# Kernel optimization log

Hardware: AMD Instinct MI355X
Metric: run time of the kernel (lower is better)

## Reference

```python
import jax, jax.numpy as jnp
import numpy as np

# Dimensions
O, D, F_LSOA = 128, 128, 64      # origins, destinations, LSOA feature dim
T, FE, H = 128, 16, 64           # max seq len, edge_feature_dim, gru_hidden
NH, NO, PH = 128, 64, 128        # node_hidden, node_out, pair_hidden
P = O * D                        # number of O-D pairs


def _mlp3(x, W1, b1, W2, b2, W3, b3):
    # Linear->ReLU->Linear->ReLU->Linear (dropout is identity in eval mode)
    h = jax.nn.relu(x @ W1 + b1)
    h = jax.nn.relu(h @ W2 + b2)
    return h @ W3 + b3


def setup_inputs() -> dict:
    key = jax.random.key(0)
    ks = jax.random.split(key, 32)

    def rn(k, shape, s):
        return jax.random.normal(k, shape, dtype=jnp.float32) * s

    inp = {
        "O_feats": rn(ks[0], (O, F_LSOA), 1.0),
        "D_feats": rn(ks[1], (D, F_LSOA), 1.0),
        "seqs": rn(ks[2], (P, T, FE), 1.0),
        "lengths": jax.random.randint(ks[3], (P,), 1, T + 1, dtype=jnp.int32),
        # enc_O
        "WO1": rn(ks[4], (F_LSOA, NH), 0.05), "bO1": jnp.zeros((NH,), jnp.float32),
        "WO2": rn(ks[5], (NH, NH), 0.05),     "bO2": jnp.zeros((NH,), jnp.float32),
        "WO3": rn(ks[6], (NH, NO), 0.05),     "bO3": jnp.zeros((NO,), jnp.float32),
        # enc_D
        "WD1": rn(ks[7], (F_LSOA, NH), 0.05), "bD1": jnp.zeros((NH,), jnp.float32),
        "WD2": rn(ks[8], (NH, NH), 0.05),     "bD2": jnp.zeros((NH,), jnp.float32),
        "WD3": rn(ks[9], (NH, NO), 0.05),     "bD3": jnp.zeros((NO,), jnp.float32),
        # pair_head: 2*node_out -> pair_hidden -> 1
        "Wp1": rn(ks[10], (2 * NO, PH), 0.05), "bp1": jnp.zeros((PH,), jnp.float32),
        "Wp2": rn(ks[11], (PH, 1), 0.05),      "bp2": jnp.zeros((1,), jnp.float32),
        # GRU (gate order r, z, n as in PyTorch)
        "W_ih": rn(ks[12], (FE, 3 * H), 0.1),  "b_ih": jnp.zeros((3 * H,), jnp.float32),
        "W_hh": rn(ks[13], (H, 3 * H), 0.1),   "b_hh": jnp.zeros((3 * H,), jnp.float32),
        # seq_head
        "Ws": rn(ks[14], (H, 1), 0.1),         "bs": jnp.zeros((1,), jnp.float32),
    }
    return inp


def reference(O_feats, D_feats, seqs, lengths,
              WO1, bO1, WO2, bO2, WO3, bO3,
              WD1, bD1, WD2, bD2, WD3, bD3,
              Wp1, bp1, Wp2, bp2,
              W_ih, W_hh, b_ih, b_hh,
              Ws, bs):
    # Node encoders
    eo = _mlp3(O_feats, WO1, bO1, WO2, bO2, WO3, bO3)   # [O, NO]
    ed = _mlp3(D_feats, WD1, bD1, WD2, bD2, WD3, bD3)   # [D, NO]

    # Pairwise score: concat(eo, ed) -> MLP -> softplus
    pair_in = jnp.concatenate([
        jnp.broadcast_to(eo[:, None, :], (O, D, NO)),
        jnp.broadcast_to(ed[None, :, :], (O, D, NO)),
    ], axis=-1)                                          # [O, D, 2*NO]
    hp = jax.nn.relu(pair_in @ Wp1 + bp1)                # [O, D, PH]
    z_pair = (hp @ Wp2 + bp2)[..., 0]                    # [O, D]
    s_pair = jax.nn.softplus(z_pair)

    # Length-masked GRU over all O*D padded sequences (equiv. to pack_padded)
    xT = jnp.swapaxes(seqs, 0, 1)                        # [T, P, FE]
    h0 = jnp.zeros((P, H), jnp.float32)

    def step(h, inp):
        xt, t = inp
        gx = xt @ W_ih + b_ih                            # [P, 3H]
        gh = h @ W_hh + b_hh                             # [P, 3H]
        xr, xz, xn = jnp.split(gx, 3, axis=-1)
        hr, hz, hn = jnp.split(gh, 3, axis=-1)
        r = jax.nn.sigmoid(xr + hr)
        zg = jax.nn.sigmoid(xz + hz)
        n = jnp.tanh(xn + r * hn)
        h_new = (1.0 - zg) * n + zg * h
        h = jnp.where((t < lengths)[:, None], h_new, h)  # freeze past seq end
        return h, None

    h_last, _ = jax.lax.scan(step, h0, (xT, jnp.arange(T)))  # [P, H]

    p_seq = jax.nn.sigmoid(h_last @ Ws + bs)[:, 0].reshape(O, D)
    return jnp.sum(s_pair * p_seq)
```

## Files before the change

### kernel.cpp

```cpp
#include <hip/hip_runtime.h>
#include <hip/hip_bf16.h>

#define O_N 128
#define D_N 128
#define F_LS 64
#define T_MAX 128
#define FE_N 16
#define H_GRU 64
#define NH 128
#define NO 64
#define PH 128
#define NG 1024

typedef _Float16 f16;
typedef f16 f16x4 __attribute__((ext_vector_type(4)));
typedef f16 f16x8 __attribute__((ext_vector_type(8)));
typedef float f32x4 __attribute__((ext_vector_type(4)));

__device__ __forceinline__ float fast_sigmoid(float x) {
    return __builtin_amdgcn_rcpf(1.f + __expf(-x));
}

__global__ __launch_bounds__(128) void k_enc(
    const float* __restrict__ O_feats, const float* __restrict__ D_feats,
    const float* __restrict__ WO1, const float* __restrict__ bO1,
    const float* __restrict__ WO2, const float* __restrict__ bO2,
    const float* __restrict__ WO3, const float* __restrict__ bO3,
    const float* __restrict__ WD1, const float* __restrict__ bD1,
    const float* __restrict__ WD2, const float* __restrict__ bD2,
    const float* __restrict__ WD3, const float* __restrict__ bD3,
    const float* __restrict__ Wp1,
    float* __restrict__ PA, float* __restrict__ PB, float* __restrict__ d_out)
{
    __shared__ float h1[NH];
    __shared__ float h2[NH];
    __shared__ float ev[NO];
    const int b = blockIdx.x;
    const int enc = b >> 7;
    const int row = b & 127;
    const int t = threadIdx.x;
    if (b == 0 && t == 0) d_out[0] = 0.f;

    const float* x  = (enc ? D_feats : O_feats) + row * F_LS;
    const float* W1 = enc ? WD1 : WO1;  const float* b1 = enc ? bD1 : bO1;
    const float* W2 = enc ? WD2 : WO2;  const float* b2 = enc ? bD2 : bO2;
    const float* W3 = enc ? WD3 : WO3;  const float* b3 = enc ? bD3 : bO3;

    float a = b1[t];
    #pragma unroll 8
    for (int k = 0; k < F_LS; ++k) a += x[k] * W1[k * NH + t];
    h1[t] = fmaxf(a, 0.f);
    __syncthreads();

    a = b2[t];
    #pragma unroll 8
    for (int k = 0; k < NH; ++k) a += h1[k] * W2[k * NH + t];
    h2[t] = fmaxf(a, 0.f);
    __syncthreads();

    if (t < NO) {
        a = b3[t];
        #pragma unroll 8
        for (int k = 0; k < NH; ++k) a += h2[k] * W3[k * NO + t];
        ev[t] = a;
    }
    __syncthreads();

    const float* Wp = Wp1 + (enc ? NO * PH : 0);
    a = 0.f;
    #pragma unroll 8
    for (int k = 0; k < NO; ++k) a += ev[k] * Wp[k * PH + t];
    (enc ? PB : PA)[row * PH + t] = a;
}

__global__ __launch_bounds__(128) void k_pair(
    const float* __restrict__ PA, const float* __restrict__ PB,
    const float* __restrict__ bp1, const float* __restrict__ Wp2,
    const float* __restrict__ bp2, float* __restrict__ s_pair)
{
    const int i = blockIdx.x;
    const int j = threadIdx.x;
    __shared__ float pa[PH];
    __shared__ float b1s[PH];
    __shared__ float w2s[PH];
    pa[j]  = PA[i * PH + j];
    b1s[j] = bp1[j];
    w2s[j] = Wp2[j];
    __syncthreads();
    const float* pb = PB + j * PH;
    float acc = 0.f;
    #pragma unroll 8
    for (int c = 0; c < PH; ++c)
        acc += w2s[c] * fmaxf(pa[c] + pb[c] + b1s[c], 0.f);
    float z = acc + bp2[0];
    float sp = fmaxf(z, 0.f) + log1pf(__expf(-fabsf(z)));
    s_pair[i * 128 + j] = sp;
}

__global__ __launch_bounds__(1024) void k_sort(
    const int* __restrict__ lengths, int* __restrict__ perm)
{
    __shared__ int cnt[130];
    __shared__ int suf[130];
    const int t = threadIdx.x;
    if (t < 130) cnt[t] = 0;
    __syncthreads();
    for (int i = t; i < 16384; i += 1024) atomicAdd(&cnt[lengths[i]], 1);
    __syncthreads();
    if (t < 130) suf[t] = cnt[t];
    __syncthreads();
    for (int d = 1; d < 130; d <<= 1) {
        int v = 0;
        if (t < 130) { v = suf[t]; if (t + d < 130) v += suf[t + d]; }
        __syncthreads();
        if (t < 130) suf[t] = v;
        __syncthreads();
    }
    if (t < 129) cnt[t] = (t + 1 < 130) ? suf[t + 1] : 0;
    __syncthreads();
    for (int i = t; i < 16384; i += 1024) {
        int pos = atomicAdd(&cnt[lengths[i]], 1);
        perm[pos] = i;
    }
}

__global__ __launch_bounds__(256, 4) void k_gru(
    const float* __restrict__ seqs, const int* __restrict__ lengths,
    const int* __restrict__ perm,
    const float* __restrict__ W_ih, const float* __restrict__ b_ih,
    const float* __restrict__ W_hh, const float* __restrict__ b_hh,
    const float* __restrict__ Ws, const float* __restrict__ bs,
    const float* __restrict__ s_pair, float* __restrict__ d_out)
{
    __shared__ __align__(16) f16 hbuf[2][16 * 72];
    __shared__ float red[64];
    const int tid = threadIdx.x;
    const int w  = tid >> 6;
    const int l  = tid & 63;
    const int q  = l >> 4;
    const int n  = l & 15;
    const int c  = w * 16 + n;
    const int colbase = w * 16 + q * 4;
    const int pb = blockIdx.x * 16;
    const float S_RZ = -1.4426950408889634f;
    const float S_N  =  2.8853900817779268f;

    f16x8 wh[3][2], wi[3];
    #pragma unroll
    for (int g = 0; g < 3; ++g) {
        const int gb = g * 64;
        const float s = (g < 2) ? S_RZ : S_N;
        #pragma unroll
        for (int ks = 0; ks < 2; ++ks)
            #pragma unroll
            for (int j = 0; j < 8; ++j)
                wh[g][ks][j] = (f16)(W_hh[(ks * 32 + q * 8 + j) * 192 + gb + c] * s);
        #pragma unroll
        for (int j = 0; j < 8; ++j) {
            int k = q * 8 + j;
            wi[g][j] = (k < FE_N) ? (f16)(W_ih[k * 192 + gb + c] * s) : (f16)0.f;
        }
    }
    f32x4 c_r, c_z, c_hn, c_xn;
    float wsc[4];
    #pragma unroll
    for (int r = 0; r < 4; ++r) {
        int col = colbase + r;
        c_r[r]  = S_RZ * (b_ih[col] + b_hh[col]);
        c_z[r]  = S_RZ * (b_ih[64 + col] + b_hh[64 + col]);
        c_hn[r] = S_N * b_hh[128 + col];
        c_xn[r] = S_N * b_ih[128 + col];
        wsc[r]  = Ws[col];
    }
    const int myp   = perm[pb + n];
    const int mylen = lengths[myp];
    int ml = mylen;
    ml = max(ml, __shfl_xor(ml, 1));
    ml = max(ml, __shfl_xor(ml, 2));
    ml = max(ml, __shfl_xor(ml, 4));
    ml = max(ml, __shfl_xor(ml, 8));
    const int maxlen = __builtin_amdgcn_readfirstlane(ml);

    {
        f16x8 z8 = {(f16)0, (f16)0, (f16)0, (f16)0, (f16)0, (f16)0, (f16)0, (f16)0};
        if (tid < 144) *(f16x8*)&hbuf[0][tid * 8] = z8;
    }

    const float4* xp = (const float4*)(seqs + (size_t)myp * (T_MAX * FE_N)) + q * 2;
    float4 xa = {0.f, 0.f, 0.f, 0.f}, xb = xa;
    if (q < 2) { xa = xp[0]; xb = xp[1]; }

    float hold[4] = {0.f, 0.f, 0.f, 0.f};
    const f16x8 zero8 = {(f16)0, (f16)0, (f16)0, (f16)0, (f16)0, (f16)0, (f16)0, (f16)0};
    __syncthreads();

    #pragma unroll 1
    for (int t = 0; t < maxlen; t += 2) {
        #pragma unroll
        for (int sub = 0; sub < 2; ++sub) {
            const int tt = t + sub;
            if (sub == 1 && tt >= maxlen) break;
            const f16* hb  = hbuf[sub];
            f16*       hbw = hbuf[sub ^ 1];

            f16x8 ax = zero8;
            if (q < 2) {
                ax[0] = (f16)xa.x; ax[1] = (f16)xa.y; ax[2] = (f16)xa.z; ax[3] = (f16)xa.w;
                ax[4] = (f16)xb.x; ax[5] = (f16)xb.y; ax[6] = (f16)xb.z; ax[7] = (f16)xb.w;
                int tn = (tt + 1 < maxlen) ? (tt + 1) : tt;
                xa = xp[tn * 4];
                xb = xp[tn * 4 + 1];
            }
            f16x8 bh0 = *(const f16x8*)&hb[n * 72 + 8 * q];
            f16x8 bh1 = *(const f16x8*)&hb[n * 72 + 32 + 8 * q];

            f32x4 ar = __builtin_amdgcn_mfma_f32_16x16x32_f16(wh[0][0], bh0, c_r, 0, 0, 0);
            ar = __builtin_amdgcn_mfma_f32_16x16x32_f16(wh[0][1], bh1, ar, 0, 0, 0);
            ar = __builtin_amdgcn_mfma_f32_16x16x32_f16(wi[0],    ax,  ar, 0, 0, 0);
            f32x4 az = __builtin_amdgcn_mfma_f32_16x16x32_f16(wh[1][0], bh0, c_z, 0, 0, 0);
            az = __builtin_amdgcn_mfma_f32_16x16x32_f16(wh[1][1], bh1, az, 0, 0, 0);
            az = __builtin_amdgcn_mfma_f32_16x16x32_f16(wi[1],    ax,  az, 0, 0, 0);
            f32x4 hn = __builtin_amdgcn_mfma_f32_16x16x32_f16(wh[2][0], bh0, c_hn, 0, 0, 0);
            hn = __builtin_amdgcn_mfma_f32_16x16x32_f16(wh[2][1], bh1, hn, 0, 0, 0);
            f32x4 xn = __builtin_amdgcn_mfma_f32_16x16x32_f16(wi[2], ax, c_xn, 0, 0, 0);

            const bool live = (tt < mylen);
            #pragma unroll
            for (int r = 0; r < 4; ++r) {
                float rg    = __builtin_amdgcn_rcpf(1.f + __builtin_amdgcn_exp2f(ar[r]));
                float zg    = __builtin_amdgcn_rcpf(1.f + __builtin_amdgcn_exp2f(az[r]));
                float inner = fmaf(rg, hn[r], xn[r]);
                float nn    = fmaf(-2.f, __builtin_amdgcn_rcpf(1.f + __builtin_amdgcn_exp2f(inner)), 1.f);
                float hnew  = fmaf(zg, hold[r] - nn, nn);
                hold[r] = live ? hnew : hold[r];
            }
            f16x4 hv4;
            hv4[0] = (f16)hold[0];
            hv4[1] = (f16)hold[1];
            hv4[2] = (f16)hold[2];
            hv4[3] = (f16)hold[3];
            *(f16x4*)&hbw[n * 72 + colbase] = hv4;
            __syncthreads();
        }
    }

    float part = hold[0] * wsc[0] + hold[1] * wsc[1] +
                 hold[2] * wsc[2] + hold[3] * wsc[3];
    part += __shfl_xor(part, 16);
    part += __shfl_xor(part, 32);
    if (l < 16) red[w * 16 + n] = part;
    __syncthreads();
    if (tid < 16) {
        float s = red[tid] + red[16 + tid] + red[32 + tid] + red[48 + tid];
        float pv = fast_sigmoid(s + bs[0]);
        float contrib = s_pair[perm[pb + tid]] * pv;
        #pragma unroll
        for (int off = 1; off < 16; off <<= 1)
            contrib += __shfl_xor(contrib, off);
        if (tid == 0) atomicAdd(d_out, contrib);
    }
}

extern "C" void kernel_launch(void* const* d_in, const int* in_sizes, int n_in,
                              void* d_out, int out_size, void* d_ws, size_t ws_size,
                              hipStream_t stream)
{
    const float* O_feats = (const float*)d_in[0];
    const float* D_feats = (const float*)d_in[1];
    const float* seqs    = (const float*)d_in[2];
    const int*   lengths = (const int*)d_in[3];
    const float* WO1 = (const float*)d_in[4];  const float* bO1 = (const float*)d_in[5];
    const float* WO2 = (const float*)d_in[6];  const float* bO2 = (const float*)d_in[7];
    const float* WO3 = (const float*)d_in[8];  const float* bO3 = (const float*)d_in[9];
    const float* WD1 = (const float*)d_in[10]; const float* bD1 = (const float*)d_in[11];
    const float* WD2 = (const float*)d_in[12]; const float* bD2 = (const float*)d_in[13];
    const float* WD3 = (const float*)d_in[14]; const float* bD3 = (const float*)d_in[15];
    const float* Wp1 = (const float*)d_in[16]; const float* bp1 = (const float*)d_in[17];
    const float* Wp2 = (const float*)d_in[18]; const float* bp2 = (const float*)d_in[19];
    const float* W_ih = (const float*)d_in[20]; const float* b_ih = (const float*)d_in[21];
    const float* W_hh = (const float*)d_in[22]; const float* b_hh = (const float*)d_in[23];
    const float* Ws   = (const float*)d_in[24]; const float* bs   = (const float*)d_in[25];

    float* out    = (float*)d_out;
    float* PA     = (float*)d_ws;
    float* PB     = PA + 128 * 128;
    float* s_pair = PB + 128 * 128;
    int*   perm   = (int*)(s_pair + 16384);

    k_enc<<<256, 128, 0, stream>>>(O_feats, D_feats,
                                   WO1, bO1, WO2, bO2, WO3, bO3,
                                   WD1, bD1, WD2, bD2, WD3, bD3,
                                   Wp1, PA, PB, out);
    k_pair<<<128, 128, 0, stream>>>(PA, PB, bp1, Wp2, bp2, s_pair);
    k_sort<<<1, 1024, 0, stream>>>(lengths, perm);
    k_gru<<<1024, 256, 0, stream>>>(seqs, lengths, perm, W_ih, b_ih, W_hh, b_hh,
                                    Ws, bs, s_pair, out);
}
```

Baseline: 367.0 us.

## Run each GRU tile in a single wavefront to drop block barriers

Moves the whole 16-sequence GRU tile into one 64-thread wavefront. Each lane now holds the weights for all four 16-column output tiles, so the per-step __syncthreads and the double-buffered LDS hidden state go away. The r/z/xn biases are folded into the input MFMA through a constant-one input element. The cost is four times the serial MFMA and activation work per wave and fewer resident waves per CU to hide MFMA and transcendental latency.

```diff
diff --git a/kernel.cpp b/kernel.cpp
--- a/kernel.cpp
+++ b/kernel.cpp
@@ -10,7 +10,6 @@
 #define NH 128
 #define NO 64
 #define PH 128
-#define NG 1024
 
 typedef _Float16 f16;
 typedef f16 f16x4 __attribute__((ext_vector_type(4)));
@@ -124,7 +123,7 @@
     }
 }
 
-__global__ __launch_bounds__(256, 4) void k_gru(
+__global__ __launch_bounds__(64, 1) void k_gru(
     const float* __restrict__ seqs, const int* __restrict__ lengths,
     const int* __restrict__ perm,
     const float* __restrict__ W_ih, const float* __restrict__ b_ih,
@@ -132,46 +131,49 @@
     const float* __restrict__ Ws, const float* __restrict__ bs,
     const float* __restrict__ s_pair, float* __restrict__ d_out)
 {
-    __shared__ __align__(16) f16 hbuf[2][16 * 72];
-    __shared__ float red[64];
+    __shared__ __align__(16) f16 hbuf[16 * 72];
     const int tid = threadIdx.x;
-    const int w  = tid >> 6;
-    const int l  = tid & 63;
-    const int q  = l >> 4;
-    const int n  = l & 15;
-    const int c  = w * 16 + n;
-    const int colbase = w * 16 + q * 4;
+    const int q = tid >> 4;
+    const int n = tid & 15;
     const int pb = blockIdx.x * 16;
     const float S_RZ = -1.4426950408889634f;
     const float S_N  =  2.8853900817779268f;
 
-    f16x8 wh[3][2], wi[3];
+    f16x8 wh[3][4][2], wi[3][4];
+    f32x4 c_hn[4];
     #pragma unroll
     for (int g = 0; g < 3; ++g) {
-        const int gb = g * 64;
         const float s = (g < 2) ? S_RZ : S_N;
         #pragma unroll
-        for (int ks = 0; ks < 2; ++ks)
+        for (int mt = 0; mt < 4; ++mt) {
+            const int col = g * 64 + mt * 16 + n;
             #pragma unroll
-            for (int j = 0; j < 8; ++j)
-                wh[g][ks][j] = (f16)(W_hh[(ks * 32 + q * 8 + j) * 192 + gb + c] * s);
-        #pragma unroll
-        for (int j = 0; j < 8; ++j) {
-            int k = q * 8 + j;
-            wi[g][j] = (k < FE_N) ? (f16)(W_ih[k * 192 + gb + c] * s) : (f16)0.f;
+            for (int ks = 0; ks < 2; ++ks)
+                #pragma unroll
+                for (int j = 0; j < 8; ++j)
+                    wh[g][mt][ks][j] = (f16)(W_hh[(ks * 32 + q * 8 + j) * 192 + col] * s);
+            #pragma unroll
+            for (int j = 0; j < 8; ++j) {
+                const int k = q * 8 + j;
+                float v = 0.f;
+                if (k < FE_N) {
+                    v = W_ih[k * 192 + col] * s;
+                } else if (k == FE_N) {
+                    const int c0 = mt * 16 + n;
+                    v = (g == 0) ? S_RZ * (b_ih[c0] + b_hh[c0])
+                      : (g == 1) ? S_RZ * (b_ih[64 + c0] + b_hh[64 + c0])
+                                 : S_N * b_ih[128 + c0];
+                }
+                wi[g][mt][j] = (f16)v;
+            }
         }
     }
-    f32x4 c_r, c_z, c_hn, c_xn;
-    float wsc[4];
     #pragma unroll
-    for (int r = 0; r < 4; ++r) {
-        int col = colbase + r;
-        c_r[r]  = S_RZ * (b_ih[col] + b_hh[col]);
-        c_z[r]  = S_RZ * (b_ih[64 + col] + b_hh[64 + col]);
-        c_hn[r] = S_N * b_hh[128 + col];
-        c_xn[r] = S_N * b_ih[128 + col];
-        wsc[r]  = Ws[col];
-    }
+    for (int mt = 0; mt < 4; ++mt)
+        #pragma unroll
+        for (int r = 0; r < 4; ++r)
+            c_hn[mt][r] = S_N * b_hh[128 + mt * 16 + q * 4 + r];
+
     const int myp   = perm[pb + n];
     const int mylen = lengths[myp];
     int ml = mylen;
@@ -182,78 +184,80 @@
     const int maxlen = __builtin_amdgcn_readfirstlane(ml);
 
     {
-        f16x8 z8 = {(f16)0, (f16)0, (f16)0, (f16)0, (f16)0, (f16)0, (f16)0, (f16)0};
-        if (tid < 144) *(f16x8*)&hbuf[0][tid * 8] = z8;
+        f16x8 z8 = {};
+        #pragma unroll
+        for (int i = 0; i < 3; ++i) {
+            int idx = tid + i * 64;
+            if (idx < 144) *(f16x8*)&hbuf[idx * 8] = z8;
+        }
     }
 
     const float4* xp = (const float4*)(seqs + (size_t)myp * (T_MAX * FE_N)) + q * 2;
-    float4 xa = {0.f, 0.f, 0.f, 0.f}, xb = xa;
-    if (q < 2) { xa = xp[0]; xb = xp[1]; }
-
-    float hold[4] = {0.f, 0.f, 0.f, 0.f};
-    const f16x8 zero8 = {(f16)0, (f16)0, (f16)0, (f16)0, (f16)0, (f16)0, (f16)0, (f16)0};
-    __syncthreads();
-
-    #pragma unroll 1
-    for (int t = 0; t < maxlen; t += 2) {
-        #pragma unroll
-        for (int sub = 0; sub < 2; ++sub) {
-            const int tt = t + sub;
-            if (sub == 1 && tt >= maxlen) break;
-            const f16* hb  = hbuf[sub];
-            f16*       hbw = hbuf[sub ^ 1];
-
-            f16x8 ax = zero8;
-            if (q < 2) {
-                ax[0] = (f16)xa.x; ax[1] = (f16)xa.y; ax[2] = (f16)xa.z; ax[3] = (f16)xa.w;
-                ax[4] = (f16)xb.x; ax[5] = (f16)xb.y; ax[6] = (f16)xb.z; ax[7] = (f16)xb.w;
-                int tn = (tt + 1 < maxlen) ? (tt + 1) : tt;
-                xa = xp[tn * 4];
-                xb = xp[tn * 4 + 1];
-            }
-            f16x8 bh0 = *(const f16x8*)&hb[n * 72 + 8 * q];
-            f16x8 bh1 = *(const f16x8*)&hb[n * 72 + 32 + 8 * q];
-
-            f32x4 ar = __builtin_amdgcn_mfma_f32_16x16x32_f16(wh[0][0], bh0, c_r, 0, 0, 0);
-            ar = __builtin_amdgcn_mfma_f32_16x16x32_f16(wh[0][1], bh1, ar, 0, 0, 0);
-            ar = __builtin_amdgcn_mfma_f32_16x16x32_f16(wi[0],    ax,  ar, 0, 0, 0);
-            f32x4 az = __builtin_amdgcn_mfma_f32_16x16x32_f16(wh[1][0], bh0, c_z, 0, 0, 0);
-            az = __builtin_amdgcn_mfma_f32_16x16x32_f16(wh[1][1], bh1, az, 0, 0, 0);
-            az = __builtin_amdgcn_mfma_f32_16x16x32_f16(wi[1],    ax,  az, 0, 0, 0);
-            f32x4 hn = __builtin_amdgcn_mfma_f32_16x16x32_f16(wh[2][0], bh0, c_hn, 0, 0, 0);
-            hn = __builtin_amdgcn_mfma_f32_16x16x32_f16(wh[2][1], bh1, hn, 0, 0, 0);
-            f32x4 xn = __builtin_amdgcn_mfma_f32_16x16x32_f16(wi[2], ax, c_xn, 0, 0, 0);
-
-            const bool live = (tt < mylen);
+    float4 x0a = {0.f, 0.f, 0.f, 0.f}, x0b = x0a, x1a = x0a, x1b = x0a;
+    if (q < 2) {
+        x0a = xp[0]; x0b = xp[1];
+        x1a = xp[4]; x1b = xp[5];
+    }
+    f16x8 ax = {};
+    if (q == 2) ax[0] = (f16)1.f;
+    const f32x4 zc = {0.f, 0.f, 0.f, 0.f};
+    float hold[4][4] = {};
+
+    auto step = [&](int TT, float4& XA, float4& XB) {
+        f16x8 bh0 = *(const f16x8*)&hbuf[n * 72 + 8 * q];
+        f16x8 bh1 = *(const f16x8*)&hbuf[n * 72 + 32 + 8 * q];
+        if (q < 2) {
+            ax[0] = (f16)XA.x; ax[1] = (f16)XA.y;
+            ax[2] = (f16)XA.z; ax[3] = (f16)XA.w;
+            ax[4] = (f16)XB.x; ax[5] = (f16)XB.y;
+            ax[6] = (f16)XB.z; ax[7] = (f16)XB.w;
+            int tn = (TT + 2 < maxlen) ? (TT + 2) : (maxlen - 1);
+            XA = xp[tn * 4]; XB = xp[tn * 4 + 1];
+        }
+        const bool live = (TT < mylen);
+        #pragma unroll
+        for (int mt = 0; mt < 4; ++mt) {
+            f32x4 ar = __builtin_amdgcn_mfma_f32_16x16x32_f16(wh[0][mt][0], bh0, zc, 0, 0, 0);
+            ar = __builtin_amdgcn_mfma_f32_16x16x32_f16(wh[0][mt][1], bh1, ar, 0, 0, 0);
+            ar = __builtin_amdgcn_mfma_f32_16x16x32_f16(wi[0][mt],    ax,  ar, 0, 0, 0);
+            f32x4 az = __builtin_amdgcn_mfma_f32_16x16x32_f16(wh[1][mt][0], bh0, zc, 0, 0, 0);
+            az = __builtin_amdgcn_mfma_f32_16x16x32_f16(wh[1][mt][1], bh1, az, 0, 0, 0);
+            az = __builtin_amdgcn_mfma_f32_16x16x32_f16(wi[1][mt],    ax,  az, 0, 0, 0);
+            f32x4 hn = __builtin_amdgcn_mfma_f32_16x16x32_f16(wh[2][mt][0], bh0, c_hn[mt], 0, 0, 0);
+            hn = __builtin_amdgcn_mfma_f32_16x16x32_f16(wh[2][mt][1], bh1, hn, 0, 0, 0);
+            f32x4 xn = __builtin_amdgcn_mfma_f32_16x16x32_f16(wi[2][mt], ax, zc, 0, 0, 0);
+            f16x4 hv4;
             #pragma unroll
             for (int r = 0; r < 4; ++r) {
                 float rg    = __builtin_amdgcn_rcpf(1.f + __builtin_amdgcn_exp2f(ar[r]));
                 float zg    = __builtin_amdgcn_rcpf(1.f + __builtin_amdgcn_exp2f(az[r]));
                 float inner = fmaf(rg, hn[r], xn[r]);
                 float nn    = fmaf(-2.f, __builtin_amdgcn_rcpf(1.f + __builtin_amdgcn_exp2f(inner)), 1.f);
-                float hnew  = fmaf(zg, hold[r] - nn, nn);
-                hold[r] = live ? hnew : hold[r];
+                float hnew  = fmaf(zg, hold[mt][r] - nn, nn);
+                hold[mt][r] = live ? hnew : hold[mt][r];
+                hv4[r] = (f16)hold[mt][r];
             }
-            f16x4 hv4;
-            hv4[0] = (f16)hold[0];
-            hv4[1] = (f16)hold[1];
-            hv4[2] = (f16)hold[2];
-            hv4[3] = (f16)hold[3];
-            *(f16x4*)&hbw[n * 72 + colbase] = hv4;
-            __syncthreads();
+            *(f16x4*)&hbuf[n * 72 + mt * 16 + 4 * q] = hv4;
         }
-    }
-
-    float part = hold[0] * wsc[0] + hold[1] * wsc[1] +
-                 hold[2] * wsc[2] + hold[3] * wsc[3];
+    };
+
+    #pragma unroll 1
+    for (int t = 0; t < maxlen; t += 2) {
+        step(t, x0a, x0b);
+        if (t + 1 < maxlen) step(t + 1, x1a, x1b);
+    }
+
+    float part = 0.f;
+    #pragma unroll
+    for (int mt = 0; mt < 4; ++mt)
+        #pragma unroll
+        for (int r = 0; r < 4; ++r)
+            part += hold[mt][r] * Ws[mt * 16 + q * 4 + r];
     part += __shfl_xor(part, 16);
     part += __shfl_xor(part, 32);
-    if (l < 16) red[w * 16 + n] = part;
-    __syncthreads();
     if (tid < 16) {
-        float s = red[tid] + red[16 + tid] + red[32 + tid] + red[48 + tid];
-        float pv = fast_sigmoid(s + bs[0]);
-        float contrib = s_pair[perm[pb + tid]] * pv;
+        float pv = fast_sigmoid(part + bs[0]);
+        float contrib = s_pair[myp] * pv;
         #pragma unroll
         for (int off = 1; off < 16; off <<= 1)
             contrib += __shfl_xor(contrib, off);
@@ -293,6 +297,6 @@
                                    Wp1, PA, PB, out);
     k_pair<<<128, 128, 0, stream>>>(PA, PB, bp1, Wp2, bp2, s_pair);
     k_sort<<<1, 1024, 0, stream>>>(lengths, perm);
-    k_gru<<<1024, 256, 0, stream>>>(seqs, lengths, perm, W_ih, b_ih, W_hh, b_hh,
-                                    Ws, bs, s_pair, out);
-}
+    k_gru<<<1024, 64, 0, stream>>>(seqs, lengths, perm, W_ih, b_ih, W_hh, b_hh,
+                                   Ws, bs, s_pair, out);
+}
```

Measured after the change: 408.2 us. 1.11x slower.

## Pack four GRU sequence groups per 1024-thread block with deeper input prefetch

Applied to the files above, without the earlier changes.

Each GRU workgroup now holds four independent 16-sequence groups: 16 waves, 1024 threads, 256 blocks. The loop is bounded by the block's longest sequence, and each group skips steps past its own sorted max length. The seqs input is now prefetched two steps ahead into separate per-sub-step registers. The input-projection MFMAs are issued before the hidden-state ones, and f16 packing uses cvt_pkrtz. The risks are that barriers now span 16 waves, so groups with shorter sequences sit idle, and that launch_bounds(1024,4) may squeeze the VGPR budget and cause spills.

```diff
diff --git a/kernel.cpp b/kernel.cpp
--- a/kernel.cpp
+++ b/kernel.cpp
@@ -10,9 +10,10 @@
 #define NH 128
 #define NO 64
 #define PH 128
-#define NG 1024
+#define ENG 4
 
 typedef _Float16 f16;
+typedef __fp16 hf2 __attribute__((ext_vector_type(2)));
 typedef f16 f16x4 __attribute__((ext_vector_type(4)));
 typedef f16 f16x8 __attribute__((ext_vector_type(8)));
 typedef float f32x4 __attribute__((ext_vector_type(4)));
@@ -124,7 +125,7 @@
     }
 }
 
-__global__ __launch_bounds__(256, 4) void k_gru(
+__global__ __launch_bounds__(1024, 4) void k_gru(
     const float* __restrict__ seqs, const int* __restrict__ lengths,
     const int* __restrict__ perm,
     const float* __restrict__ W_ih, const float* __restrict__ b_ih,
@@ -132,16 +133,18 @@
     const float* __restrict__ Ws, const float* __restrict__ bs,
     const float* __restrict__ s_pair, float* __restrict__ d_out)
 {
-    __shared__ __align__(16) f16 hbuf[2][16 * 72];
-    __shared__ float red[64];
+    __shared__ __align__(16) f16 hbuf[ENG][2][16 * 72];
+    __shared__ float red[ENG][64];
     const int tid = threadIdx.x;
-    const int w  = tid >> 6;
+    const int wave = tid >> 6;
+    const int e = wave >> 2;
+    const int wi_ = wave & 3;
     const int l  = tid & 63;
     const int q  = l >> 4;
     const int n  = l & 15;
-    const int c  = w * 16 + n;
-    const int colbase = w * 16 + q * 4;
-    const int pb = blockIdx.x * 16;
+    const int c  = wi_ * 16 + n;
+    const int colbase = wi_ * 16 + q * 4;
+    const int pb = blockIdx.x * 64 + e * 16;
     const float S_RZ = -1.4426950408889634f;
     const float S_N  =  2.8853900817779268f;
 
@@ -174,90 +177,93 @@
     }
     const int myp   = perm[pb + n];
     const int mylen = lengths[myp];
-    int ml = mylen;
-    ml = max(ml, __shfl_xor(ml, 1));
-    ml = max(ml, __shfl_xor(ml, 2));
-    ml = max(ml, __shfl_xor(ml, 4));
-    ml = max(ml, __shfl_xor(ml, 8));
-    const int maxlen = __builtin_amdgcn_readfirstlane(ml);
+    const int elen  = lengths[perm[pb]];
+    const int blen  = lengths[perm[blockIdx.x * 64]];
 
     {
-        f16x8 z8 = {(f16)0, (f16)0, (f16)0, (f16)0, (f16)0, (f16)0, (f16)0, (f16)0};
-        if (tid < 144) *(f16x8*)&hbuf[0][tid * 8] = z8;
+        f16x8 z8 = {};
+        f16* hb = (f16*)hbuf;
+        #pragma unroll 2
+        for (int i = tid; i < 1152; i += 1024) *(f16x8*)&hb[i * 8] = z8;
     }
 
     const float4* xp = (const float4*)(seqs + (size_t)myp * (T_MAX * FE_N)) + q * 2;
-    float4 xa = {0.f, 0.f, 0.f, 0.f}, xb = xa;
-    if (q < 2) { xa = xp[0]; xb = xp[1]; }
-
+    float4 x0a = {0.f, 0.f, 0.f, 0.f}, x0b = x0a, x1a = x0a, x1b = x0a;
+    if (q < 2) {
+        x0a = xp[0]; x0b = xp[1];
+        x1a = xp[4]; x1b = xp[5];
+    }
+    f16x8 ax = {};
     float hold[4] = {0.f, 0.f, 0.f, 0.f};
-    const f16x8 zero8 = {(f16)0, (f16)0, (f16)0, (f16)0, (f16)0, (f16)0, (f16)0, (f16)0};
-    __syncthreads();
+    __syncthreads();
+
+    auto step = [&](int TT, int sub, float4& XA, float4& XB) {
+        const f16* hb  = hbuf[e][sub];
+        f16*       hbw = hbuf[e][sub ^ 1];
+        f16x8 bh0 = *(const f16x8*)&hb[n * 72 + 8 * q];
+        f16x8 bh1 = *(const f16x8*)&hb[n * 72 + 32 + 8 * q];
+        if (q < 2) {
+            union { f16x8 v8; hf2 v2[4]; } u;
+            u.v2[0] = __builtin_amdgcn_cvt_pkrtz(XA.x, XA.y);
+            u.v2[1] = __builtin_amdgcn_cvt_pkrtz(XA.z, XA.w);
+            u.v2[2] = __builtin_amdgcn_cvt_pkrtz(XB.x, XB.y);
+            u.v2[3] = __builtin_amdgcn_cvt_pkrtz(XB.z, XB.w);
+            ax = u.v8;
+            int tn = (TT + 2 < elen) ? (TT + 2) : (elen - 1);
+            XA = xp[tn * 4]; XB = xp[tn * 4 + 1];
+        }
+        f32x4 ar = __builtin_amdgcn_mfma_f32_16x16x32_f16(wi[0], ax, c_r, 0, 0, 0);
+        f32x4 az = __builtin_amdgcn_mfma_f32_16x16x32_f16(wi[1], ax, c_z, 0, 0, 0);
+        f32x4 xn = __builtin_amdgcn_mfma_f32_16x16x32_f16(wi[2], ax, c_xn, 0, 0, 0);
+        ar = __builtin_amdgcn_mfma_f32_16x16x32_f16(wh[0][0], bh0, ar, 0, 0, 0);
+        ar = __builtin_amdgcn_mfma_f32_16x16x32_f16(wh[0][1], bh1, ar, 0, 0, 0);
+        az = __builtin_amdgcn_mfma_f32_16x16x32_f16(wh[1][0], bh0, az, 0, 0, 0);
+        az = __builtin_amdgcn_mfma_f32_16x16x32_f16(wh[1][1], bh1, az, 0, 0, 0);
+        f32x4 hn = __builtin_amdgcn_mfma_f32_16x16x32_f16(wh[2][0], bh0, c_hn, 0, 0, 0);
+        hn = __builtin_amdgcn_mfma_f32_16x16x32_f16(wh[2][1], bh1, hn, 0, 0, 0);
+
+        const bool live = (TT < mylen);
+        #pragma unroll
+        for (int r = 0; r < 4; ++r) {
+            float rg    = __builtin_amdgcn_rcpf(1.f + __builtin_amdgcn_exp2f(ar[r]));
+            float zg    = __builtin_amdgcn_rcpf(1.f + __builtin_amdgcn_exp2f(az[r]));
+            float inner = fmaf(rg, hn[r], xn[r]);
+            float nn    = fmaf(-2.f, __builtin_amdgcn_rcpf(1.f + __builtin_amdgcn_exp2f(inner)), 1.f);
+            float hnew  = fmaf(zg, hold[r] - nn, nn);
+            hold[r] = live ? hnew : hold[r];
+        }
+        union { f16x4 v4; hf2 v2[2]; } hu;
+        hu.v2[0] = __builtin_amdgcn_cvt_pkrtz(hold[0], hold[1]);
+        hu.v2[1] = __builtin_amdgcn_cvt_pkrtz(hold[2], hold[3]);
+        *(f16x4*)&hbw[n * 72 + colbase] = hu.v4;
+    };
 
     #pragma unroll 1
-    for (int t = 0; t < maxlen; t += 2) {
-        #pragma unroll
-        for (int sub = 0; sub < 2; ++sub) {
-            const int tt = t + sub;
-            if (sub == 1 && tt >= maxlen) break;
-            const f16* hb  = hbuf[sub];
-            f16*       hbw = hbuf[sub ^ 1];
-
-            f16x8 ax = zero8;
-            if (q < 2) {
-                ax[0] = (f16)xa.x; ax[1] = (f16)xa.y; ax[2] = (f16)xa.z; ax[3] = (f16)xa.w;
-                ax[4] = (f16)xb.x; ax[5] = (f16)xb.y; ax[6] = (f16)xb.z; ax[7] = (f16)xb.w;
-                int tn = (tt + 1 < maxlen) ? (tt + 1) : tt;
-                xa = xp[tn * 4];
-                xb = xp[tn * 4 + 1];
-            }
-            f16x8 bh0 = *(const f16x8*)&hb[n * 72 + 8 * q];
-            f16x8 bh1 = *(const f16x8*)&hb[n * 72 + 32 + 8 * q];
-
-            f32x4 ar = __builtin_amdgcn_mfma_f32_16x16x32_f16(wh[0][0], bh0, c_r, 0, 0, 0);
-            ar = __builtin_amdgcn_mfma_f32_16x16x32_f16(wh[0][1], bh1, ar, 0, 0, 0);
-            ar = __builtin_amdgcn_mfma_f32_16x16x32_f16(wi[0],    ax,  ar, 0, 0, 0);
-            f32x4 az = __builtin_amdgcn_mfma_f32_16x16x32_f16(wh[1][0], bh0, c_z, 0, 0, 0);
-            az = __builtin_amdgcn_mfma_f32_16x16x32_f16(wh[1][1], bh1, az, 0, 0, 0);
-            az = __builtin_amdgcn_mfma_f32_16x16x32_f16(wi[1],    ax,  az, 0, 0, 0);
-            f32x4 hn = __builtin_amdgcn_mfma_f32_16x16x32_f16(wh[2][0], bh0, c_hn, 0, 0, 0);
-            hn = __builtin_amdgcn_mfma_f32_16x16x32_f16(wh[2][1], bh1, hn, 0, 0, 0);
-            f32x4 xn = __builtin_amdgcn_mfma_f32_16x16x32_f16(wi[2], ax, c_xn, 0, 0, 0);
-
-            const bool live = (tt < mylen);
-            #pragma unroll
-            for (int r = 0; r < 4; ++r) {
-                float rg    = __builtin_amdgcn_rcpf(1.f + __builtin_amdgcn_exp2f(ar[r]));
-                float zg    = __builtin_amdgcn_rcpf(1.f + __builtin_amdgcn_exp2f(az[r]));
-                float inner = fmaf(rg, hn[r], xn[r]);
-                float nn    = fmaf(-2.f, __builtin_amdgcn_rcpf(1.f + __builtin_amdgcn_exp2f(inner)), 1.f);
-                float hnew  = fmaf(zg, hold[r] - nn, nn);
-                hold[r] = live ? hnew : hold[r];
-            }
-            f16x4 hv4;
-            hv4[0] = (f16)hold[0];
-            hv4[1] = (f16)hold[1];
-            hv4[2] = (f16)hold[2];
-            hv4[3] = (f16)hold[3];
-            *(f16x4*)&hbw[n * 72 + colbase] = hv4;
-            __syncthreads();
-        }
+    for (int t = 0; t < blen; t += 2) {
+        if (t < elen) step(t, 0, x0a, x0b);
+        __syncthreads();
+        if (t + 1 >= blen) break;
+        if (t + 1 < elen) step(t + 1, 1, x1a, x1b);
+        __syncthreads();
     }
 
     float part = hold[0] * wsc[0] + hold[1] * wsc[1] +
                  hold[2] * wsc[2] + hold[3] * wsc[3];
     part += __shfl_xor(part, 16);
     part += __shfl_xor(part, 32);
-    if (l < 16) red[w * 16 + n] = part;
-    __syncthreads();
-    if (tid < 16) {
-        float s = red[tid] + red[16 + tid] + red[32 + tid] + red[48 + tid];
+    if (l < 16) red[e][wi_ * 16 + n] = part;
+    __syncthreads();
+    if (tid < 64) {
+        const int eo = tid >> 4;
+        const int nn_ = tid & 15;
+        float s = red[eo][nn_] + red[eo][16 + nn_] + red[eo][32 + nn_] + red[eo][48 + nn_];
         float pv = fast_sigmoid(s + bs[0]);
-        float contrib = s_pair[perm[pb + tid]] * pv;
-        #pragma unroll
-        for (int off = 1; off < 16; off <<= 1)
-            contrib += __shfl_xor(contrib, off);
-        if (tid == 0) atomicAdd(d_out, contrib);
+        float contrib = s_pair[perm[blockIdx.x * 64 + eo * 16 + nn_]] * pv;
+        contrib += __shfl_xor(contrib, 1);
+        contrib += __shfl_xor(contrib, 2);
+        contrib += __shfl_xor(contrib, 4);
+        contrib += __shfl_xor(contrib, 8);
+        if (nn_ == 0) atomicAdd(d_out, contrib);
     }
 }
 
@@ -293,6 +299,6 @@
                                    Wp1, PA, PB, out);
     k_pair<<<128, 128, 0, stream>>>(PA, PB, bp1, Wp2, bp2, s_pair);
     k_sort<<<1, 1024, 0, stream>>>(lengths, perm);
-    k_gru<<<1024, 256, 0, stream>>>(seqs, lengths, perm, W_ih, b_ih, W_hh, b_hh,
+    k_gru<<<256, 1024, 0, stream>>>(seqs, lengths, perm, W_ih, b_ih, W_hh, b_hh,
                                     Ws, bs, s_pair, out);
 }
```

Result: slower. 378.9 us (+3.2%).

## Prefetch GRU inputs two steps ahead, reorder MFMAs, interleave block mapping, transpose PB

Applied to the files above, without the earlier changes.

The GRU step now keeps two input register buffers and prefetches each input two timesteps ahead. It also issues the input-projection MFMAs before the hidden-state MFMAs, so the global load latency and the LDS hidden-state read are hidden better. Block indices are remapped so that consecutive launched blocks take groups spread across the length-sorted permutation, which evens out work between CUs and waves. The pair head stores PB transposed with bp1 folded in, giving coalesced reads in k_pair, and f16 packing uses cvt_pkrtz (round toward zero), which slightly changes rounding.

```diff
diff --git a/kernel.cpp b/kernel.cpp
--- a/kernel.cpp
+++ b/kernel.cpp
@@ -10,9 +10,9 @@
 #define NH 128
 #define NO 64
 #define PH 128
-#define NG 1024
 
 typedef _Float16 f16;
+typedef __fp16 hf2 __attribute__((ext_vector_type(2)));
 typedef f16 f16x4 __attribute__((ext_vector_type(4)));
 typedef f16 f16x8 __attribute__((ext_vector_type(8)));
 typedef float f32x4 __attribute__((ext_vector_type(4)));
@@ -29,8 +29,8 @@
     const float* __restrict__ WD1, const float* __restrict__ bD1,
     const float* __restrict__ WD2, const float* __restrict__ bD2,
     const float* __restrict__ WD3, const float* __restrict__ bD3,
-    const float* __restrict__ Wp1,
-    float* __restrict__ PA, float* __restrict__ PB, float* __restrict__ d_out)
+    const float* __restrict__ Wp1, const float* __restrict__ bp1,
+    float* __restrict__ PA, float* __restrict__ PBt, float* __restrict__ d_out)
 {
     __shared__ float h1[NH];
     __shared__ float h2[NH];
@@ -70,28 +70,26 @@
     a = 0.f;
     #pragma unroll 8
     for (int k = 0; k < NO; ++k) a += ev[k] * Wp[k * PH + t];
-    (enc ? PB : PA)[row * PH + t] = a;
+    if (enc) PBt[t * 128 + row] = a + bp1[t];
+    else     PA[row * PH + t] = a;
 }
 
 __global__ __launch_bounds__(128) void k_pair(
-    const float* __restrict__ PA, const float* __restrict__ PB,
-    const float* __restrict__ bp1, const float* __restrict__ Wp2,
-    const float* __restrict__ bp2, float* __restrict__ s_pair)
+    const float* __restrict__ PA, const float* __restrict__ PBt,
+    const float* __restrict__ Wp2, const float* __restrict__ bp2,
+    float* __restrict__ s_pair)
 {
     const int i = blockIdx.x;
     const int j = threadIdx.x;
     __shared__ float pa[PH];
-    __shared__ float b1s[PH];
     __shared__ float w2s[PH];
     pa[j]  = PA[i * PH + j];
-    b1s[j] = bp1[j];
     w2s[j] = Wp2[j];
     __syncthreads();
-    const float* pb = PB + j * PH;
     float acc = 0.f;
     #pragma unroll 8
     for (int c = 0; c < PH; ++c)
-        acc += w2s[c] * fmaxf(pa[c] + pb[c] + b1s[c], 0.f);
+        acc += w2s[c] * fmaxf(pa[c] + PBt[c * 128 + j], 0.f);
     float z = acc + bp2[0];
     float sp = fmaxf(z, 0.f) + log1pf(__expf(-fabsf(z)));
     s_pair[i * 128 + j] = sp;
@@ -141,24 +139,25 @@
     const int n  = l & 15;
     const int c  = w * 16 + n;
     const int colbase = w * 16 + q * 4;
-    const int pb = blockIdx.x * 16;
+    const int g  = (blockIdx.x & 255) * 4 + (blockIdx.x >> 8);
+    const int pb = g * 16;
     const float S_RZ = -1.4426950408889634f;
     const float S_N  =  2.8853900817779268f;
 
     f16x8 wh[3][2], wi[3];
     #pragma unroll
-    for (int g = 0; g < 3; ++g) {
-        const int gb = g * 64;
-        const float s = (g < 2) ? S_RZ : S_N;
+    for (int gg = 0; gg < 3; ++gg) {
+        const int gb = gg * 64;
+        const float s = (gg < 2) ? S_RZ : S_N;
         #pragma unroll
         for (int ks = 0; ks < 2; ++ks)
             #pragma unroll
             for (int j = 0; j < 8; ++j)
-                wh[g][ks][j] = (f16)(W_hh[(ks * 32 + q * 8 + j) * 192 + gb + c] * s);
+                wh[gg][ks][j] = (f16)(W_hh[(ks * 32 + q * 8 + j) * 192 + gb + c] * s);
         #pragma unroll
         for (int j = 0; j < 8; ++j) {
             int k = q * 8 + j;
-            wi[g][j] = (k < FE_N) ? (f16)(W_ih[k * 192 + gb + c] * s) : (f16)0.f;
+            wi[gg][j] = (k < FE_N) ? (f16)(W_ih[k * 192 + gb + c] * s) : (f16)0.f;
         }
     }
     f32x4 c_r, c_z, c_hn, c_xn;
@@ -182,66 +181,68 @@
     const int maxlen = __builtin_amdgcn_readfirstlane(ml);
 
     {
-        f16x8 z8 = {(f16)0, (f16)0, (f16)0, (f16)0, (f16)0, (f16)0, (f16)0, (f16)0};
+        f16x8 z8 = {};
         if (tid < 144) *(f16x8*)&hbuf[0][tid * 8] = z8;
     }
 
     const float4* xp = (const float4*)(seqs + (size_t)myp * (T_MAX * FE_N)) + q * 2;
-    float4 xa = {0.f, 0.f, 0.f, 0.f}, xb = xa;
-    if (q < 2) { xa = xp[0]; xb = xp[1]; }
-
+    float4 x0a = {0.f, 0.f, 0.f, 0.f}, x0b = x0a, x1a = x0a, x1b = x0a;
+    if (q < 2) {
+        x0a = xp[0]; x0b = xp[1];
+        x1a = xp[4]; x1b = xp[5];
+    }
+    f16x8 ax = {};
     float hold[4] = {0.f, 0.f, 0.f, 0.f};
-    const f16x8 zero8 = {(f16)0, (f16)0, (f16)0, (f16)0, (f16)0, (f16)0, (f16)0, (f16)0};
-    __syncthreads();
+    __syncthreads();
+
+    auto step = [&](int TT, int sub, float4& XA, float4& XB) {
+        const f16* hb  = hbuf[sub];
+        f16*       hbw = hbuf[sub ^ 1];
+        f16x8 bh0 = *(const f16x8*)&hb[n * 72 + 8 * q];
+        f16x8 bh1 = *(const f16x8*)&hb[n * 72 + 32 + 8 * q];
+        if (q < 2) {
+            union { f16x8 v8; hf2 v2[4]; } u;
+            u.v2[0] = __builtin_amdgcn_cvt_pkrtz(XA.x, XA.y);
+            u.v2[1] = __builtin_amdgcn_cvt_pkrtz(XA.z, XA.w);
+            u.v2[2] = __builtin_amdgcn_cvt_pkrtz(XB.x, XB.y);
+            u.v2[3] = __builtin_amdgcn_cvt_pkrtz(XB.z, XB.w);
+            ax = u.v8;
+            int tn = (TT + 2 < maxlen) ? (TT + 2) : (maxlen - 1);
+            XA = xp[tn * 4]; XB = xp[tn * 4 + 1];
+        }
+        f32x4 ar = __builtin_amdgcn_mfma_f32_16x16x32_f16(wi[0], ax, c_r, 0, 0, 0);
+        f32x4 az = __builtin_amdgcn_mfma_f32_16x16x32_f16(wi[1], ax, c_z, 0, 0, 0);
+        f32x4 xn = __builtin_amdgcn_mfma_f32_16x16x32_f16(wi[2], ax, c_xn, 0, 0, 0);
+        ar = __builtin_amdgcn_mfma_f32_16x16x32_f16(wh[0][0], bh0, ar, 0, 0, 0);
+        ar = __builtin_amdgcn_mfma_f32_16x16x32_f16(wh[0][1], bh1, ar, 0, 0, 0);
+        az = __builtin_amdgcn_mfma_f32_16x16x32_f16(wh[1][0], bh0, az, 0, 0, 0);
+        az = __builtin_amdgcn_mfma_f32_16x16x32_f16(wh[1][1], bh1, az, 0, 0, 0);
+        f32x4 hn = __builtin_amdgcn_mfma_f32_16x16x32_f16(wh[2][0], bh0, c_hn, 0, 0, 0);
+        hn = __builtin_amdgcn_mfma_f32_16x16x32_f16(wh[2][1], bh1, hn, 0, 0, 0);
+
+        const bool live = (TT < mylen);
+        #pragma unroll
+        for (int r = 0; r < 4; ++r) {
+            float rg    = __builtin_amdgcn_rcpf(1.f + __builtin_amdgcn_exp2f(ar[r]));
+            float zg    = __builtin_amdgcn_rcpf(1.f + __builtin_amdgcn_exp2f(az[r]));
+            float inner = fmaf(rg, hn[r], xn[r]);
+            float nn    = fmaf(-2.f, __builtin_amdgcn_rcpf(1.f + __builtin_amdgcn_exp2f(inner)), 1.f);
+            float hnew  = fmaf(zg, hold[r] - nn, nn);
+            hold[r] = live ? hnew : hold[r];
+        }
+        union { f16x4 v4; hf2 v2[2]; } hu;
+        hu.v2[0] = __builtin_amdgcn_cvt_pkrtz(hold[0], hold[1]);
+        hu.v2[1] = __builtin_amdgcn_cvt_pkrtz(hold[2], hold[3]);
+        *(f16x4*)&hbw[n * 72 + colbase] = hu.v4;
+    };
 
     #pragma unroll 1
     for (int t = 0; t < maxlen; t += 2) {
-        #pragma unroll
-        for (int sub = 0; sub < 2; ++sub) {
-            const int tt = t + sub;
-            if (sub == 1 && tt >= maxlen) break;
-            const f16* hb  = hbuf[sub];
-            f16*       hbw = hbuf[sub ^ 1];
-
-            f16x8 ax = zero8;
-            if (q < 2) {
-                ax[0] = (f16)xa.x; ax[1] = (f16)xa.y; ax[2] = (f16)xa.z; ax[3] = (f16)xa.w;
-                ax[4] = (f16)xb.x; ax[5] = (f16)xb.y; ax[6] = (f16)xb.z; ax[7] = (f16)xb.w;
-                int tn = (tt + 1 < maxlen) ? (tt + 1) : tt;
-                xa = xp[tn * 4];
-                xb = xp[tn * 4 + 1];
-            }
-            f16x8 bh0 = *(const f16x8*)&hb[n * 72 + 8 * q];
-            f16x8 bh1 = *(const f16x8*)&hb[n * 72 + 32 + 8 * q];
-
-            f32x4 ar = __builtin_amdgcn_mfma_f32_16x16x32_f16(wh[0][0], bh0, c_r, 0, 0, 0);
-            ar = __builtin_amdgcn_mfma_f32_16x16x32_f16(wh[0][1], bh1, ar, 0, 0, 0);
-            ar = __builtin_amdgcn_mfma_f32_16x16x32_f16(wi[0],    ax,  ar, 0, 0, 0);
-            f32x4 az = __builtin_amdgcn_mfma_f32_16x16x32_f16(wh[1][0], bh0, c_z, 0, 0, 0);
-            az = __builtin_amdgcn_mfma_f32_16x16x32_f16(wh[1][1], bh1, az, 0, 0, 0);
-            az = __builtin_amdgcn_mfma_f32_16x16x32_f16(wi[1],    ax,  az, 0, 0, 0);
-            f32x4 hn = __builtin_amdgcn_mfma_f32_16x16x32_f16(wh[2][0], bh0, c_hn, 0, 0, 0);
-            hn = __builtin_amdgcn_mfma_f32_16x16x32_f16(wh[2][1], bh1, hn, 0, 0, 0);
-            f32x4 xn = __builtin_amdgcn_mfma_f32_16x16x32_f16(wi[2], ax, c_xn, 0, 0, 0);
-
-            const bool live = (tt < mylen);
-            #pragma unroll
-            for (int r = 0; r < 4; ++r) {
-                float rg    = __builtin_amdgcn_rcpf(1.f + __builtin_amdgcn_exp2f(ar[r]));
-                float zg    = __builtin_amdgcn_rcpf(1.f + __builtin_amdgcn_exp2f(az[r]));
-                float inner = fmaf(rg, hn[r], xn[r]);
-                float nn    = fmaf(-2.f, __builtin_amdgcn_rcpf(1.f + __builtin_amdgcn_exp2f(inner)), 1.f);
-                float hnew  = fmaf(zg, hold[r] - nn, nn);
-                hold[r] = live ? hnew : hold[r];
-            }
-            f16x4 hv4;
-            hv4[0] = (f16)hold[0];
-            hv4[1] = (f16)hold[1];
-            hv4[2] = (f16)hold[2];
-            hv4[3] = (f16)hold[3];
-            *(f16x4*)&hbw[n * 72 + colbase] = hv4;
-            __syncthreads();
-        }
+        step(t, 0, x0a, x0b);
+        __syncthreads();
+        if (t + 1 >= maxlen) break;
+        step(t + 1, 1, x1a, x1b);
+        __syncthreads();
     }
 
     float part = hold[0] * wsc[0] + hold[1] * wsc[1] +
@@ -283,15 +284,15 @@
 
     float* out    = (float*)d_out;
     float* PA     = (float*)d_ws;
-    float* PB     = PA + 128 * 128;
-    float* s_pair = PB + 128 * 128;
+    float* PBt    = PA + 128 * 128;
+    float* s_pair = PBt + 128 * 128;
     int*   perm   = (int*)(s_pair + 16384);
 
     k_enc<<<256, 128, 0, stream>>>(O_feats, D_feats,
                                    WO1, bO1, WO2, bO2, WO3, bO3,
                                    WD1, bD1, WD2, bD2, WD3, bD3,
-                                   Wp1, PA, PB, out);
-    k_pair<<<128, 128, 0, stream>>>(PA, PB, bp1, Wp2, bp2, s_pair);
+                                   Wp1, bp1, PA, PBt, out);
+    k_pair<<<128, 128, 0, stream>>>(PA, PBt, Wp2, bp2, s_pair);
     k_sort<<<1, 1024, 0, stream>>>(lengths, perm);
     k_gru<<<1024, 256, 0, stream>>>(seqs, lengths, perm, W_ih, b_ih, W_hh, b_hh,
                                     Ws, bs, s_pair, out);
```

Result: slower. 384.4 us (+4.8%).
